# Kernel tuning notes

Measured on AMD Instinct MI355X. Metric: run time of the kernel, lower is better.

Reference implementation:

```python
import jax, jax.numpy as jnp
import numpy as np

CLIP = 100000.0


def heaviside(x):
    # smooth heaviside surrogate used by the layer
    return (jnp.tanh(10.0 * x) + 1.0) * 0.5


def evapotranspiration(wu, wl, wd, pet):
    et1 = heaviside(wu - pet) * pet + heaviside(pet - wu) * wu
    rem = heaviside(0.0 - (pet - et1)) * 0.0 + heaviside(pet - et1) * (pet - et1)
    et22 = heaviside(rem - wl) * wl + heaviside(wl - rem) * rem
    et2 = heaviside(rem) * et22
    et33 = heaviside(rem - et2 - wd) * wd + heaviside(wd - (rem - et2)) * (rem - et2)
    et3 = heaviside(rem - et2) * et33
    return et1, et2, et3


def runoff_production(wu, wl, wd, p, wum, wlm, wdm, b, c):
    wum = wum * 19.9 + 0.1
    wlm = wlm * 30.0 + 60.0
    wdm = wdm * 60.0 + 60.0
    c = c * 0.19 + 0.01
    b = b * 0.3 + 0.1
    w_total = wum + wlm + wdm
    s = c * (wu / w_total) ** 2 + b * (wl / w_total) ** 2
    return heaviside(p - s) * (p - s)


def water_source_partition(runoff, k1, k2, k3):
    k1 = k1 * 0.69 + 0.01
    k2 = k2 * 0.69 + 0.01
    k3 = k3 * 0.89 + 0.01
    surface = k1 * runoff
    interflow = k2 * (runoff - surface)
    baseflow = k3 * (runoff - surface - interflow)
    return surface, interflow, baseflow


def flow_routing(surface, interflow, baseflow):
    return surface + 0.5 * interflow + 0.25 * baseflow


def xaj_forward(inputs, wum, wlm, wdm, c, b, k1, k2, k3):
    # inputs: (B, T, 3) channels = [pet, tmean, p]
    pet_seq = inputs[:, :, 0:1]
    p_seq = inputs[:, :, 2:3]

    B = inputs.shape[0]
    # time-major driver: (T, B, 2) = [pet, p] per step (tmean unused in step)
    xs = jnp.moveaxis(jnp.stack([inputs[:, :, 0], inputs[:, :, 2]], axis=-1), 1, 0)

    def step(state, xt):
        # state: (B, 3) = [wu, wl, wd]; xt: (B, 2) = [pet, p]
        wu, wl, wd = state[:, 0], state[:, 1], state[:, 2]
        pet, p = xt[:, 0], xt[:, 1]
        et1, et2, et3 = evapotranspiration(wu, wl, wd, pet)
        wu_n = wu + jnp.clip(p - et1, -CLIP, CLIP)
        wl_n = wl + jnp.clip(p - et1 - et2, -CLIP, CLIP)
        wd_n = wd + jnp.clip(p - et1 - et2 - et3, -CLIP, CLIP)
        ns = jnp.stack([wu_n, wl_n, wd_n], axis=1)
        return ns, ns

    init = jnp.zeros((B, 3), dtype=inputs.dtype)
    _, traj = jax.lax.scan(step, init, xs)           # (T, B, 3)
    outputs = jnp.moveaxis(traj, 0, 1)               # (B, T, 3)

    wu = outputs[:, :, 0:1]
    wl = outputs[:, :, 1:2]
    wd = outputs[:, :, 2:3]

    # NOTE: original call site passes (wu, wd, wl, ...) and (wum, wdm, wlm, ...)
    # positionally into runoff_production -- replicated faithfully.
    runoff = runoff_production(wu, wd, wl, p_seq, wum, wdm, wlm, b, c)
    surface, interflow, baseflow = water_source_partition(runoff, k1, k2, k3)
    total_q = flow_routing(surface, interflow, baseflow)  # (B, T, 1)
    return total_q


def setup_inputs() -> dict:
    key = jax.random.key(0)
    ks = jax.random.split(key, 9)
    B, T = 4096, 2048
    inp = {"inputs": jax.random.uniform(ks[0], (B, T, 3), dtype=jnp.float32)}
    for i, name in enumerate(["wum", "wlm", "wdm", "c", "b", "k1", "k2", "k3"]):
        inp[name] = jax.random.uniform(ks[i + 1], (1,), dtype=jnp.float32)
    return inp


def reference(inputs, wum, wlm, wdm, c, b, k1, k2, k3):
    return xaj_forward(inputs, wum, wlm, wdm, c, b, k1, k2, k3)
```

## Files before the change

kernel.cpp:

```cpp
#include <hip/hip_runtime.h>

typedef float f32x4 __attribute__((ext_vector_type(4)));

#define T_LEN 2048
#define GROUP 16
#define NG    (T_LEN / GROUP)
#define NT    (NG + 3)
#define CH    12
#define KH    28.853901f

__device__ __forceinline__ float hs_neg(float negKx) {
    float e = __builtin_amdgcn_exp2f(negKx);
    return __builtin_amdgcn_rcpf(1.0f + e);
}

#define WAITV(N) asm volatile("s_waitcnt vmcnt(" #N ")" ::: "memory")
#define TICK_BARRIER() do {                                   \
    asm volatile("s_waitcnt lgkmcnt(0)" ::: "memory");        \
    __builtin_amdgcn_s_barrier();                             \
    __builtin_amdgcn_sched_barrier(0); } while (0)

#define DMA_GROUP(SLOT, G) do {                                                \
    const float* g_ = row + (size_t)(G) * (3 * GROUP);                         \
    _Pragma("unroll")                                                          \
    for (int j_ = 0; j_ < CH; ++j_) {                                          \
        __builtin_amdgcn_global_load_lds(                                      \
            (const __attribute__((address_space(1))) void*)(g_ + 4 * j_),      \
            (__attribute__((address_space(3))) void*)&s_in[SLOT][j_][0],       \
            16, 0, 0);                                                         \
    } } while (0)

__global__ __launch_bounds__(256, 1)
void xaj_pipe_kernel(const float* __restrict__ inp,
                     const float* __restrict__ p_wum,
                     const float* __restrict__ p_wlm,
                     const float* __restrict__ p_wdm,
                     const float* __restrict__ p_c,
                     const float* __restrict__ p_b,
                     const float* __restrict__ p_k1,
                     const float* __restrict__ p_k2,
                     const float* __restrict__ p_k3,
                     float* __restrict__ out)
{
    __shared__ f32x4 s_in [6][CH][64];
    __shared__ float s_rem[2][GROUP][64];
    __shared__ float s_d1 [2][GROUP][64];
    __shared__ float s_wu [4][GROUP][64];
    __shared__ float s_u  [2][GROUP][64];
    __shared__ float s_d2 [2][GROUP][64];
    __shared__ float s_wd [2][GROUP][64];

    const int lane  = threadIdx.x & 63;
    const int wv    = threadIdx.x >> 6;
    const int chain = blockIdx.x * 64 + lane;
    const float* __restrict__ row = inp + (size_t)chain * (3 * T_LEN);
    float* __restrict__ orow      = out + (size_t)chain * T_LEN;

    const float wum = p_wum[0], wlm = p_wlm[0], wdm = p_wdm[0];
    const float cc  = p_c[0],   bb  = p_b[0];
    const float k1  = p_k1[0],  k2  = p_k2[0],  k3 = p_k3[0];

    const float w_total = (wum * 19.9f + 0.1f)
                        + (wdm * 30.0f + 60.0f)
                        + (wlm * 60.0f + 60.0f);
    const float inv_wt = 1.0f / w_total;
    const float c_s = cc * 0.19f + 0.01f;
    const float b_s = bb * 0.3f  + 0.1f;
    const float k1s = k1 * 0.69f + 0.01f;
    const float k2s = k2 * 0.69f + 0.01f;
    const float k3s = k3 * 0.89f + 0.01f;
    const float Kq = k1s + 0.5f * k2s * (1.0f - k1s)
                   + 0.25f * k3s * (1.0f - k1s) * (1.0f - k2s);

    float st = 0.0f;

    if (wv == 0) {
        DMA_GROUP(0, 0);
        DMA_GROUP(1, 1);
    }

    for (int t = 0; t < NT; ++t) {
        if (wv == 0) {
            if (t < NG) {
                if (t < NG - 1) { WAITV(12); } else { WAITV(0); }
                f32x4 fv[CH];
                const int s6 = t % 6;
#pragma unroll
                for (int j = 0; j < CH; ++j) fv[j] = s_in[s6][j][lane];
                if (t + 2 < NG) DMA_GROUP((t + 2) % 6, t + 2);
#pragma unroll
                for (int j = 0; j < GROUP; ++j) {
                    float pet = fv[(3*j)   >> 2][(3*j)   & 3];
                    float p   = fv[(3*j+2) >> 2][(3*j+2) & 3];
                    float dwp = pet - st;
                    float a   = hs_neg(KH * dwp);
                    float et1 = fmaf(a, dwp, st);
                    float x   = pet - et1;
                    float hx  = hs_neg(fmaf(KH, et1, -KH * pet));
                    float rem = hx * x;
                    float d1  = p - et1;
                    st = fmaf(-a, dwp, p);
                    s_rem[t & 1][j][lane] = rem;
                    s_d1 [t & 1][j][lane] = d1;
                    s_wu [t & 3][j][lane] = st;
                }
            }
        } else if (wv == 1) {
            const int g = t - 1;
            if (g >= 0 && g < NG) {
#pragma unroll
                for (int j = 0; j < GROUP; ++j) {
                    float rem  = s_rem[g & 1][j][lane];
                    float d1   = s_d1 [g & 1][j][lane];
                    float nKr  = -KH * rem;
                    float b2   = hs_neg(fmaf(KH, st, nKr));
                    float hrem = hs_neg(nKr);
                    float et22 = fmaf(b2, st - rem, rem);
                    float et2  = hrem * et22;
                    float u    = rem - et2;
                    float d2   = d1 - et2;
                    float wld1 = st + d1;
                    st = fmaf(-hrem, et22, wld1);
                    s_u [g & 1][j][lane] = u;
                    s_d2[g & 1][j][lane] = d2;
                }
            }
        } else if (wv == 2) {
            const int g = t - 2;
            if (g >= 0 && g < NG) {
#pragma unroll
                for (int j = 0; j < GROUP; ++j) {
                    float u    = s_u [g & 1][j][lane];
                    float d2   = s_d2[g & 1][j][lane];
                    float nKu  = -KH * u;
                    float c2   = hs_neg(fmaf(KH, st, nKu));
                    float hu   = hs_neg(nKu);
                    float et33 = fmaf(c2, st - u, u);
                    float wdd2 = st + d2;
                    st = fmaf(-hu, et33, wdd2);
                    s_wd[g & 1][j][lane] = st;
                }
            }
        } else {
            const int g = t - 3;
            if (g >= 0) {
                float qv[GROUP];
                const float* pin = (const float*)&s_in[g % 6][0][0];
#pragma unroll
                for (int j = 0; j < GROUP; ++j) {
                    float wuv = s_wu[g & 3][j][lane];
                    float wdv = s_wd[g & 1][j][lane];
                    const int f = 3 * j + 2;
                    float p  = pin[(f >> 2) * 256 + lane * 4 + (f & 3)];
                    float ru = wuv * inv_wt;
                    float rd = wdv * inv_wt;
                    float s2 = fmaf(c_s * ru, ru, (b_s * rd) * rd);
                    float ps = p - s2;
                    qv[j] = hs_neg(-KH * ps) * ps * Kq;
                }
                f32x4* o4 = (f32x4*)(orow + (size_t)g * GROUP);
#pragma unroll
                for (int i = 0; i < GROUP / 4; ++i) {
                    f32x4 q = {qv[4*i], qv[4*i+1], qv[4*i+2], qv[4*i+3]};
                    o4[i] = q;
                }
            }
        }
        TICK_BARRIER();
    }
}

extern "C" void kernel_launch(void* const* d_in, const int* in_sizes, int n_in,
                              void* d_out, int out_size, void* d_ws, size_t ws_size,
                              hipStream_t stream) {
    const float* inp = (const float*)d_in[0];
    const int B = out_size / T_LEN;
    dim3 block(256), grid(B / 64);
    xaj_pipe_kernel<<<grid, block, 0, stream>>>(
        inp,
        (const float*)d_in[1],
        (const float*)d_in[2],
        (const float*)d_in[3],
        (const float*)d_in[4],
        (const float*)d_in[5],
        (const float*)d_in[6],
        (const float*)d_in[7],
        (const float*)d_in[8],
        (float*)d_out);
}
```

Before: 137.1 us.

## Replace lockstep barrier pipeline with LDS flag-based producer/consumer handoff between waves

Drops the per-tick workgroup barrier that forced all four wavefront stages into lockstep and replaces it with per-stage progress counters in shared memory that each wave polls with s_sleep. Each stage now waits only on its upstream producer and on the downstream consumer freeing a buffer, so stages can drift relative to one another. It also shrinks the input ring to three slots, stages precipitation into its own buffer for the output wave, and trims the et1/rem arithmetic. The cost is spin-polling on volatile LDS flags with sleep latency, plus ordering that depends on lgkmcnt waits and compiler fences being correct.

New measurement: 225.5 us. 1.65x slower.

```diff
diff --git a/kernel.cpp b/kernel.cpp
--- a/kernel.cpp
+++ b/kernel.cpp
@@ -5,7 +5,6 @@
 #define T_LEN 2048
 #define GROUP 16
 #define NG    (T_LEN / GROUP)
-#define NT    (NG + 3)
 #define CH    12
 #define KH    28.853901f
 
@@ -15,10 +14,15 @@
 }
 
 #define WAITV(N) asm volatile("s_waitcnt vmcnt(" #N ")" ::: "memory")
-#define TICK_BARRIER() do {                                   \
-    asm volatile("s_waitcnt lgkmcnt(0)" ::: "memory");        \
-    __builtin_amdgcn_s_barrier();                             \
-    __builtin_amdgcn_sched_barrier(0); } while (0)
+#define CFENCE() asm volatile("" ::: "memory")
+
+__device__ __forceinline__ void wait_ge(volatile int* f, int val) {
+    while (*f < val) __builtin_amdgcn_s_sleep(1);
+}
+__device__ __forceinline__ void publish(volatile int* f, int val) {
+    asm volatile("s_waitcnt lgkmcnt(0)" ::: "memory");
+    *f = val;
+}
 
 #define DMA_GROUP(SLOT, G) do {                                                \
     const float* g_ = row + (size_t)(G) * (3 * GROUP);                         \
@@ -31,7 +35,7 @@
     } } while (0)
 
 __global__ __launch_bounds__(256, 1)
-void xaj_pipe_kernel(const float* __restrict__ inp,
+void xaj_flag_kernel(const float* __restrict__ inp,
                      const float* __restrict__ p_wum,
                      const float* __restrict__ p_wlm,
                      const float* __restrict__ p_wdm,
@@ -42,13 +46,15 @@
                      const float* __restrict__ p_k3,
                      float* __restrict__ out)
 {
-    __shared__ f32x4 s_in [6][CH][64];
+    __shared__ f32x4 s_in [3][CH][64];
     __shared__ float s_rem[2][GROUP][64];
     __shared__ float s_d1 [2][GROUP][64];
-    __shared__ float s_wu [4][GROUP][64];
     __shared__ float s_u  [2][GROUP][64];
     __shared__ float s_d2 [2][GROUP][64];
     __shared__ float s_wd [2][GROUP][64];
+    __shared__ float s_wu [4][GROUP][64];
+    __shared__ float s_p  [4][GROUP][64];
+    __shared__ int   s_c[4];
 
     const int lane  = threadIdx.x & 63;
     const int wv    = threadIdx.x >> 6;
@@ -72,101 +78,121 @@
     const float Kq = k1s + 0.5f * k2s * (1.0f - k1s)
                    + 0.25f * k3s * (1.0f - k1s) * (1.0f - k2s);
 
-    float st = 0.0f;
+    if (threadIdx.x < 4) s_c[threadIdx.x] = 0;
+    __syncthreads();
+
+    volatile int* vc = s_c;
 
     if (wv == 0) {
+        float wu = 0.0f;
         DMA_GROUP(0, 0);
         DMA_GROUP(1, 1);
-    }
-
-    for (int t = 0; t < NT; ++t) {
-        if (wv == 0) {
-            if (t < NG) {
-                if (t < NG - 1) { WAITV(12); } else { WAITV(0); }
-                f32x4 fv[CH];
-                const int s6 = t % 6;
-#pragma unroll
-                for (int j = 0; j < CH; ++j) fv[j] = s_in[s6][j][lane];
-                if (t + 2 < NG) DMA_GROUP((t + 2) % 6, t + 2);
-#pragma unroll
-                for (int j = 0; j < GROUP; ++j) {
-                    float pet = fv[(3*j)   >> 2][(3*j)   & 3];
-                    float p   = fv[(3*j+2) >> 2][(3*j+2) & 3];
-                    float dwp = pet - st;
-                    float a   = hs_neg(KH * dwp);
-                    float et1 = fmaf(a, dwp, st);
-                    float x   = pet - et1;
-                    float hx  = hs_neg(fmaf(KH, et1, -KH * pet));
-                    float rem = hx * x;
-                    float d1  = p - et1;
-                    st = fmaf(-a, dwp, p);
-                    s_rem[t & 1][j][lane] = rem;
-                    s_d1 [t & 1][j][lane] = d1;
-                    s_wu [t & 3][j][lane] = st;
-                }
-            }
-        } else if (wv == 1) {
-            const int g = t - 1;
-            if (g >= 0 && g < NG) {
-#pragma unroll
-                for (int j = 0; j < GROUP; ++j) {
-                    float rem  = s_rem[g & 1][j][lane];
-                    float d1   = s_d1 [g & 1][j][lane];
-                    float nKr  = -KH * rem;
-                    float b2   = hs_neg(fmaf(KH, st, nKr));
-                    float hrem = hs_neg(nKr);
-                    float et22 = fmaf(b2, st - rem, rem);
-                    float et2  = hrem * et22;
-                    float u    = rem - et2;
-                    float d2   = d1 - et2;
-                    float wld1 = st + d1;
-                    st = fmaf(-hrem, et22, wld1);
-                    s_u [g & 1][j][lane] = u;
-                    s_d2[g & 1][j][lane] = d2;
-                }
-            }
-        } else if (wv == 2) {
-            const int g = t - 2;
-            if (g >= 0 && g < NG) {
-#pragma unroll
-                for (int j = 0; j < GROUP; ++j) {
-                    float u    = s_u [g & 1][j][lane];
-                    float d2   = s_d2[g & 1][j][lane];
-                    float nKu  = -KH * u;
-                    float c2   = hs_neg(fmaf(KH, st, nKu));
-                    float hu   = hs_neg(nKu);
-                    float et33 = fmaf(c2, st - u, u);
-                    float wdd2 = st + d2;
-                    st = fmaf(-hu, et33, wdd2);
-                    s_wd[g & 1][j][lane] = st;
-                }
-            }
-        } else {
-            const int g = t - 3;
-            if (g >= 0) {
-                float qv[GROUP];
-                const float* pin = (const float*)&s_in[g % 6][0][0];
-#pragma unroll
-                for (int j = 0; j < GROUP; ++j) {
-                    float wuv = s_wu[g & 3][j][lane];
-                    float wdv = s_wd[g & 1][j][lane];
-                    const int f = 3 * j + 2;
-                    float p  = pin[(f >> 2) * 256 + lane * 4 + (f & 3)];
-                    float ru = wuv * inv_wt;
-                    float rd = wdv * inv_wt;
-                    float s2 = fmaf(c_s * ru, ru, (b_s * rd) * rd);
-                    float ps = p - s2;
-                    qv[j] = hs_neg(-KH * ps) * ps * Kq;
-                }
-                f32x4* o4 = (f32x4*)(orow + (size_t)g * GROUP);
-#pragma unroll
-                for (int i = 0; i < GROUP / 4; ++i) {
-                    f32x4 q = {qv[4*i], qv[4*i+1], qv[4*i+2], qv[4*i+3]};
-                    o4[i] = q;
-                }
-            }
-        }
-        TICK_BARRIER();
+        for (int g = 0; g < NG; ++g) {
+            if (g >= 2) wait_ge(vc + 1, g - 1);
+            if (g >= 4) wait_ge(vc + 3, g - 3);
+            if (g < NG - 1) { WAITV(12); } else { WAITV(0); }
+            CFENCE();
+            if (g + 2 < NG) DMA_GROUP((g + 2) % 3, g + 2);
+            f32x4 fv[CH];
+            const int s3 = g % 3;
+#pragma unroll
+            for (int j = 0; j < CH; ++j) fv[j] = s_in[s3][j][lane];
+#pragma unroll
+            for (int j = 0; j < GROUP; ++j) {
+                float pet = fv[(3*j)   >> 2][(3*j)   & 3];
+                float p   = fv[(3*j+2) >> 2][(3*j+2) & 3];
+                float dwp = pet - wu;
+                float a   = hs_neg(KH * dwp);
+                float y   = dwp - a * dwp;
+                float hx  = hs_neg(-KH * y);
+                float rem = hx * y;
+                float wun = fmaf(-a, dwp, p);
+                float d1  = wun - wu;
+                wu = wun;
+                s_rem[g & 1][j][lane] = rem;
+                s_d1 [g & 1][j][lane] = d1;
+                s_wu [g & 3][j][lane] = wun;
+                s_p  [g & 3][j][lane] = p;
+            }
+            publish(vc + 0, g + 1);
+        }
+    } else if (wv == 1) {
+        float wl = 0.0f;
+        for (int g = 0; g < NG; ++g) {
+            wait_ge(vc + 0, g + 1);
+            if (g >= 2) wait_ge(vc + 2, g - 1);
+            CFENCE();
+            float remv[GROUP], d1v[GROUP];
+#pragma unroll
+            for (int j = 0; j < GROUP; ++j) {
+                remv[j] = s_rem[g & 1][j][lane];
+                d1v [j] = s_d1 [g & 1][j][lane];
+            }
+#pragma unroll
+            for (int j = 0; j < GROUP; ++j) {
+                float rem  = remv[j], d1 = d1v[j];
+                float nKr  = -KH * rem;
+                float b2   = hs_neg(fmaf(KH, wl, nKr));
+                float hrem = hs_neg(nKr);
+                float et22 = fmaf(b2, wl - rem, rem);
+                float et2  = hrem * et22;
+                float wld1 = wl + d1;
+                wl = fmaf(-hrem, et22, wld1);
+                s_u [g & 1][j][lane] = rem - et2;
+                s_d2[g & 1][j][lane] = d1 - et2;
+            }
+            publish(vc + 1, g + 1);
+        }
+    } else if (wv == 2) {
+        float wd = 0.0f;
+        for (int g = 0; g < NG; ++g) {
+            wait_ge(vc + 1, g + 1);
+            if (g >= 2) wait_ge(vc + 3, g - 1);
+            CFENCE();
+            float uv[GROUP], d2v[GROUP];
+#pragma unroll
+            for (int j = 0; j < GROUP; ++j) {
+                uv [j] = s_u [g & 1][j][lane];
+                d2v[j] = s_d2[g & 1][j][lane];
+            }
+#pragma unroll
+            for (int j = 0; j < GROUP; ++j) {
+                float u   = uv[j], d2 = d2v[j];
+                float nKu = -KH * u;
+                float c2  = hs_neg(fmaf(KH, wd, nKu));
+                float hu  = hs_neg(nKu);
+                float et33 = fmaf(c2, wd - u, u);
+                float wdd2 = wd + d2;
+                wd = fmaf(-hu, et33, wdd2);
+                s_wd[g & 1][j][lane] = wd;
+            }
+            publish(vc + 2, g + 1);
+        }
+    } else {
+        for (int g = 0; g < NG; ++g) {
+            wait_ge(vc + 2, g + 1);
+            CFENCE();
+            float qv[GROUP];
+#pragma unroll
+            for (int j = 0; j < GROUP; ++j) {
+                float wuv = s_wu[g & 3][j][lane];
+                float wdv = s_wd[g & 1][j][lane];
+                float p   = s_p [g & 3][j][lane];
+                float ru = wuv * inv_wt;
+                float rd = wdv * inv_wt;
+                float s2 = fmaf(c_s * ru, ru, (b_s * rd) * rd);
+                float ps = p - s2;
+                float so = hs_neg(-KH * ps);
+                qv[j] = ps * so * Kq;
+            }
+            f32x4* o4 = (f32x4*)(orow + (size_t)g * GROUP);
+#pragma unroll
+            for (int i = 0; i < GROUP / 4; ++i) {
+                f32x4 q = {qv[4*i], qv[4*i+1], qv[4*i+2], qv[4*i+3]};
+                o4[i] = q;
+            }
+            publish(vc + 3, g + 1);
+        }
     }
 }
 
@@ -176,7 +202,7 @@
     const float* inp = (const float*)d_in[0];
     const int B = out_size / T_LEN;
     dim3 block(256), grid(B / 64);
-    xaj_pipe_kernel<<<grid, block, 0, stream>>>(
+    xaj_flag_kernel<<<grid, block, 0, stream>>>(
         inp,
         (const float*)d_in[1],
         (const float*)d_in[2],
```

## Double group size, pre-scale state by KH, and pack wu/p as fp16 for output stage

Applied to the files above, without the earlier changes.

Doubles the per-tick group to 32 timesteps, halving the number of barrier ticks, and restructures input DMA into 3 rotating 48-float chunk slots. The recurrences now carry state pre-multiplied by the heaviside constant, which removes multiplies from the serial dependency chains. The output stage reads wu and p packed as fp16 pairs instead of re-reading the input buffer. The fp16 packing of the KH-scaled state and precipitation loses precision, which may exceed the tolerance, and the larger group raises register and LDS pressure.

New measurement: 134.4 us, median of 2. No clear change (-1.9%).

```diff
diff --git a/kernel.cpp b/kernel.cpp
--- a/kernel.cpp
+++ b/kernel.cpp
@@ -1,29 +1,30 @@
 #include <hip/hip_runtime.h>
 
-typedef float f32x4 __attribute__((ext_vector_type(4)));
+typedef float  f32x4 __attribute__((ext_vector_type(4)));
+typedef __fp16 f16x2 __attribute__((ext_vector_type(2)));
 
 #define T_LEN 2048
-#define GROUP 16
+#define GROUP 32
 #define NG    (T_LEN / GROUP)
 #define NT    (NG + 3)
-#define CH    12
 #define KH    28.853901f
 
-__device__ __forceinline__ float hs_neg(float negKx) {
-    float e = __builtin_amdgcn_exp2f(negKx);
+__device__ __forceinline__ float hs_neg(float z) {
+    float e = __builtin_amdgcn_exp2f(z);
     return __builtin_amdgcn_rcpf(1.0f + e);
 }
 
 #define WAITV(N) asm volatile("s_waitcnt vmcnt(" #N ")" ::: "memory")
+#define WAITL()  asm volatile("s_waitcnt lgkmcnt(0)" ::: "memory")
 #define TICK_BARRIER() do {                                   \
     asm volatile("s_waitcnt lgkmcnt(0)" ::: "memory");        \
     __builtin_amdgcn_s_barrier();                             \
     __builtin_amdgcn_sched_barrier(0); } while (0)
 
-#define DMA_GROUP(SLOT, G) do {                                                \
-    const float* g_ = row + (size_t)(G) * (3 * GROUP);                         \
+#define DMA_CHUNK(SLOT, C) do {                                                \
+    const float* g_ = row + (size_t)(C) * 48;                                  \
     _Pragma("unroll")                                                          \
-    for (int j_ = 0; j_ < CH; ++j_) {                                          \
+    for (int j_ = 0; j_ < 12; ++j_) {                                          \
         __builtin_amdgcn_global_load_lds(                                      \
             (const __attribute__((address_space(1))) void*)(g_ + 4 * j_),      \
             (__attribute__((address_space(3))) void*)&s_in[SLOT][j_][0],       \
@@ -31,24 +32,24 @@
     } } while (0)
 
 __global__ __launch_bounds__(256, 1)
-void xaj_pipe_kernel(const float* __restrict__ inp,
-                     const float* __restrict__ p_wum,
-                     const float* __restrict__ p_wlm,
-                     const float* __restrict__ p_wdm,
-                     const float* __restrict__ p_c,
-                     const float* __restrict__ p_b,
-                     const float* __restrict__ p_k1,
-                     const float* __restrict__ p_k2,
-                     const float* __restrict__ p_k3,
-                     float* __restrict__ out)
+void xaj_k32_kernel(const float* __restrict__ inp,
+                    const float* __restrict__ p_wum,
+                    const float* __restrict__ p_wlm,
+                    const float* __restrict__ p_wdm,
+                    const float* __restrict__ p_c,
+                    const float* __restrict__ p_b,
+                    const float* __restrict__ p_k1,
+                    const float* __restrict__ p_k2,
+                    const float* __restrict__ p_k3,
+                    float* __restrict__ out)
 {
-    __shared__ f32x4 s_in [6][CH][64];
-    __shared__ float s_rem[2][GROUP][64];
-    __shared__ float s_d1 [2][GROUP][64];
-    __shared__ float s_wu [4][GROUP][64];
-    __shared__ float s_u  [2][GROUP][64];
-    __shared__ float s_d2 [2][GROUP][64];
-    __shared__ float s_wd [2][GROUP][64];
+    __shared__ f32x4        s_in  [3][12][64];
+    __shared__ float        s_krem[2][GROUP][64];
+    __shared__ float        s_kd1 [2][GROUP][64];
+    __shared__ float        s_ku  [2][GROUP][64];
+    __shared__ float        s_kd2 [2][GROUP][64];
+    __shared__ float        s_kwd [2][GROUP][64];
+    __shared__ unsigned int s_wup [4][GROUP][64];
 
     const int lane  = threadIdx.x & 63;
     const int wv    = threadIdx.x >> 6;
@@ -71,92 +72,111 @@
     const float k3s = k3 * 0.89f + 0.01f;
     const float Kq = k1s + 0.5f * k2s * (1.0f - k1s)
                    + 0.25f * k3s * (1.0f - k1s) * (1.0f - k2s);
-
-    float st = 0.0f;
-
-    if (wv == 0) {
-        DMA_GROUP(0, 0);
-        DMA_GROUP(1, 1);
-    }
-
-    for (int t = 0; t < NT; ++t) {
+    const float C1 = inv_wt / KH;
+
+    float Kst = 0.0f;
+    int s0 = 0, s1 = 1, s2 = 2;
+
+    if (wv == 0) { DMA_CHUNK(0, 0); DMA_CHUNK(1, 1); }
+
+#pragma clang loop unroll(disable)
+    for (int T = 0; T < NT; ++T) {
         if (wv == 0) {
-            if (t < NG) {
-                if (t < NG - 1) { WAITV(12); } else { WAITV(0); }
-                f32x4 fv[CH];
-                const int s6 = t % 6;
-#pragma unroll
-                for (int j = 0; j < CH; ++j) fv[j] = s_in[s6][j][lane];
-                if (t + 2 < NG) DMA_GROUP((t + 2) % 6, t + 2);
-#pragma unroll
-                for (int j = 0; j < GROUP; ++j) {
-                    float pet = fv[(3*j)   >> 2][(3*j)   & 3];
-                    float p   = fv[(3*j+2) >> 2][(3*j+2) & 3];
-                    float dwp = pet - st;
-                    float a   = hs_neg(KH * dwp);
-                    float et1 = fmaf(a, dwp, st);
-                    float x   = pet - et1;
-                    float hx  = hs_neg(fmaf(KH, et1, -KH * pet));
-                    float rem = hx * x;
-                    float d1  = p - et1;
-                    st = fmaf(-a, dwp, p);
-                    s_rem[t & 1][j][lane] = rem;
-                    s_d1 [t & 1][j][lane] = d1;
-                    s_wu [t & 3][j][lane] = st;
-                }
+            if (T < NG) {
+                const int g = T;
+                WAITV(0);
+                f32x4 fv[24];
+#pragma unroll
+                for (int j = 0; j < 12; ++j) fv[j]      = s_in[s0][j][lane];
+#pragma unroll
+                for (int j = 0; j < 12; ++j) fv[12 + j] = s_in[s1][j][lane];
+                WAITL();
+                __builtin_amdgcn_sched_barrier(0);
+                const int c2 = 2 * g + 2, c3 = 2 * g + 3;
+                if (c2 < 2 * NG) DMA_CHUNK(s2, c2);
+                if (c3 < 2 * NG) DMA_CHUNK(s0, c3);
+                float Kwu = Kst;
+#pragma unroll
+                for (int j = 0; j < GROUP; ++j) {
+                    const int k0 = 3 * j, k2i = 3 * j + 2;
+                    float pet = fv[k0 >> 2][k0 & 3];
+                    float p   = fv[k2i >> 2][k2i & 3];
+                    float KHpet = KH * pet, Kp = KH * p;
+                    float arg  = KHpet - Kwu;
+                    float a    = hs_neg(arg);
+                    float Kwun = fmaf(-arg, a, Kp);
+                    float Kd1  = Kwun - Kwu;
+                    float Ky   = arg + (Kwun - Kp);
+                    float hx   = hs_neg(-Ky);
+                    float Krem = hx * Ky;
+                    s_krem[g & 1][j][lane] = Krem;
+                    s_kd1 [g & 1][j][lane] = Kd1;
+                    f16x2 pk = __builtin_amdgcn_cvt_pkrtz(Kwun, p);
+                    s_wup[g & 3][j][lane] = __builtin_bit_cast(unsigned int, pk);
+                    Kwu = Kwun;
+                }
+                Kst = Kwu;
+                int t0 = s0; s0 = s2; s2 = s1; s1 = t0;
             }
         } else if (wv == 1) {
-            const int g = t - 1;
-            if (g >= 0 && g < NG) {
-#pragma unroll
-                for (int j = 0; j < GROUP; ++j) {
-                    float rem  = s_rem[g & 1][j][lane];
-                    float d1   = s_d1 [g & 1][j][lane];
-                    float nKr  = -KH * rem;
-                    float b2   = hs_neg(fmaf(KH, st, nKr));
-                    float hrem = hs_neg(nKr);
-                    float et22 = fmaf(b2, st - rem, rem);
-                    float et2  = hrem * et22;
-                    float u    = rem - et2;
-                    float d2   = d1 - et2;
-                    float wld1 = st + d1;
-                    st = fmaf(-hrem, et22, wld1);
-                    s_u [g & 1][j][lane] = u;
-                    s_d2[g & 1][j][lane] = d2;
-                }
+            if (T >= 1 && T <= NG) {
+                const int g = T - 1;
+                float Kwl = Kst;
+#pragma unroll
+                for (int j = 0; j < GROUP; ++j) {
+                    float Krem = s_krem[g & 1][j][lane];
+                    float Kd1  = s_kd1 [g & 1][j][lane];
+                    float hrem = hs_neg(-Krem);
+                    float S    = Kwl + Kd1;
+                    float A    = fmaf(-hrem, Krem, S);
+                    float arg  = Kwl - Krem;
+                    float b2   = hs_neg(arg);
+                    float harg = hrem * arg;
+                    float Kwln = fmaf(-b2, harg, A);
+                    float Ket2 = S - Kwln;
+                    s_ku [g & 1][j][lane] = Krem - Ket2;
+                    s_kd2[g & 1][j][lane] = Kd1 - Ket2;
+                    Kwl = Kwln;
+                }
+                Kst = Kwl;
             }
         } else if (wv == 2) {
-            const int g = t - 2;
-            if (g >= 0 && g < NG) {
-#pragma unroll
-                for (int j = 0; j < GROUP; ++j) {
-                    float u    = s_u [g & 1][j][lane];
-                    float d2   = s_d2[g & 1][j][lane];
-                    float nKu  = -KH * u;
-                    float c2   = hs_neg(fmaf(KH, st, nKu));
-                    float hu   = hs_neg(nKu);
-                    float et33 = fmaf(c2, st - u, u);
-                    float wdd2 = st + d2;
-                    st = fmaf(-hu, et33, wdd2);
-                    s_wd[g & 1][j][lane] = st;
-                }
+            if (T >= 2 && T <= NG + 1) {
+                const int g = T - 2;
+                float Kwd = Kst;
+#pragma unroll
+                for (int j = 0; j < GROUP; ++j) {
+                    float Ku  = s_ku [g & 1][j][lane];
+                    float Kd2 = s_kd2[g & 1][j][lane];
+                    float hu  = hs_neg(-Ku);
+                    float S2  = Kwd + Kd2;
+                    float A2  = fmaf(-hu, Ku, S2);
+                    float arg = Kwd - Ku;
+                    float c2v = hs_neg(arg);
+                    float harg = hu * arg;
+                    float Kwdn = fmaf(-c2v, harg, A2);
+                    s_kwd[g & 1][j][lane] = Kwdn;
+                    Kwd = Kwdn;
+                }
+                Kst = Kwd;
             }
         } else {
-            const int g = t - 3;
-            if (g >= 0) {
+            if (T >= 3) {
+                const int g = T - 3;
                 float qv[GROUP];
-                const float* pin = (const float*)&s_in[g % 6][0][0];
-#pragma unroll
-                for (int j = 0; j < GROUP; ++j) {
-                    float wuv = s_wu[g & 3][j][lane];
-                    float wdv = s_wd[g & 1][j][lane];
-                    const int f = 3 * j + 2;
-                    float p  = pin[(f >> 2) * 256 + lane * 4 + (f & 3)];
-                    float ru = wuv * inv_wt;
-                    float rd = wdv * inv_wt;
-                    float s2 = fmaf(c_s * ru, ru, (b_s * rd) * rd);
-                    float ps = p - s2;
-                    qv[j] = hs_neg(-KH * ps) * ps * Kq;
+#pragma unroll
+                for (int j = 0; j < GROUP; ++j) {
+                    unsigned int pw = s_wup[g & 3][j][lane];
+                    f16x2 pk = __builtin_bit_cast(f16x2, pw);
+                    float Kwu_ = (float)pk[0];
+                    float p    = (float)pk[1];
+                    float Kwd_ = s_kwd[g & 1][j][lane];
+                    float ru = Kwu_ * C1;
+                    float rd = Kwd_ * C1;
+                    float s2v = fmaf(c_s * ru, ru, (b_s * rd) * rd);
+                    float ps = p - s2v;
+                    float so = hs_neg(-KH * ps);
+                    qv[j] = ps * so * Kq;
                 }
                 f32x4* o4 = (f32x4*)(orow + (size_t)g * GROUP);
 #pragma unroll
@@ -176,7 +196,7 @@
     const float* inp = (const float*)d_in[0];
     const int B = out_size / T_LEN;
     dim3 block(256), grid(B / 64);
-    xaj_pipe_kernel<<<grid, block, 0, stream>>>(
+    xaj_k32_kernel<<<grid, block, 0, stream>>>(
         inp,
         (const float*)d_in[1],
         (const float*)d_in[2],
```
